# Performance work log

Measured on AMD Instinct MI355X. Metric: run time of the kernel, lower is better.

The kernel has to match this reference:

```python
import jax, jax.numpy as jnp
import numpy as np

TEMPERATURE = 12.5      # EMDLayer temperature
SINKHORN_EPS = 0.05     # entropic regularization for the batched EMD solve
SINKHORN_ITERS = 50     # fixed iteration count (jit-friendly)
WEIGHT_EPS = 1e-05      # OpenCVSolver adds 1e-5 after relu


def setup_inputs() -> dict:
    key = jax.random.key(0)
    k1, k2, k3 = jax.random.split(key, 3)
    E, Q, W, N = 4, 75, 5, 64
    similarity_map = jax.random.uniform(k1, (E, Q, W, N, N), dtype=jnp.float32)
    weight_1 = jax.random.uniform(k2, (E, Q, W, N), dtype=jnp.float32)
    weight_2 = jax.random.uniform(k3, (E, W, Q, N), dtype=jnp.float32)
    return {"similarity_map": similarity_map, "weight_1": weight_1, "weight_2": weight_2}


def _emd_flow(cost, a, b):
    """Batched entropic-regularized EMD (log-domain Sinkhorn).
    cost: [B, N, N]; a, b: [B, N] positive marginals (each sums to N).
    Returns flow: [B, N, N] with row sums ~a and col sums ~b."""
    logK = -cost / SINKHORN_EPS            # [B, N, N]
    log_a = jnp.log(a)
    log_b = jnp.log(b)

    def step(carry, _):
        log_u, log_v = carry
        log_u = log_a - jax.scipy.special.logsumexp(logK + log_v[:, None, :], axis=2)
        log_v = log_b - jax.scipy.special.logsumexp(logK + log_u[:, :, None], axis=1)
        return (log_u, log_v), None

    init = (jnp.zeros_like(log_a), jnp.zeros_like(log_b))
    (log_u, log_v), _ = jax.lax.scan(step, init, None, length=SINKHORN_ITERS)
    return jnp.exp(logK + log_u[:, :, None] + log_v[:, None, :])


def reference(similarity_map, weight_1, weight_2):
    E, Q, W, N, _ = similarity_map.shape
    sim = similarity_map.reshape(-1, N, N)                       # [B, N, N]
    w1 = weight_1.reshape(-1, N)                                  # [B, N]
    w2 = jnp.transpose(weight_2, (0, 2, 1, 3)).reshape(-1, N)     # transpose(1,2) then flatten

    # OpenCVSolver weight preprocessing: relu + eps, renormalize to sum N
    w1 = jax.nn.relu(w1) + WEIGHT_EPS
    w1 = w1 * (N / jnp.sum(w1, axis=1, keepdims=True))
    w2 = jax.nn.relu(w2) + WEIGHT_EPS
    w2 = w2 * (N / jnp.sum(w2, axis=1, keepdims=True))

    cost = 1.0 - sim
    flow = _emd_flow(cost, w1, w2)                                # [B, N, N]
    scores = jnp.sum(flow * sim, axis=(-1, -2)).reshape(E, Q, W)
    return scores * (TEMPERATURE / N)
```

## Files before the change

### kernel.cpp

```cpp
#include <hip/hip_runtime.h>

#define N 64
#define NPAD 65
#define ITERS 50
#define TEMP 12.5f
#define WEPS 1e-5f
#define QDIM 75
#define WDIM 5

__device__ __forceinline__ float rl(float x, int lane) {
    return __int_as_float(__builtin_amdgcn_readlane(__float_as_int(x), lane));
}

__device__ __forceinline__ float waveReduceSum(float x) {
#pragma unroll
    for (int off = 32; off; off >>= 1) x += __shfl_xor(x, off, 64);
    return x;
}

__global__ __launch_bounds__(64, 1) void emd_sinkhorn_kernel(
    const float* __restrict__ sim,
    const float* __restrict__ w1,
    const float* __restrict__ w2,
    float* __restrict__ out,
    int B)
{
    __shared__ float S[N * NPAD];

    const int b    = blockIdx.x;
    const int lane = threadIdx.x;
    const float* g = sim + (size_t)b * N * N;

    const float4* g4 = (const float4*)g;
#pragma unroll
    for (int t = 0; t < 16; ++t) {
        float4 x = g4[t * 64 + lane];
        int idx = t * 64 + lane;
        int r = idx >> 4;
        int c = (idx & 15) * 4;
        S[r * NPAD + c + 0] = x.x;
        S[r * NPAD + c + 1] = x.y;
        S[r * NPAD + c + 2] = x.z;
        S[r * NPAD + c + 3] = x.w;
    }
    __syncthreads();

    float Krow[N], Kcol[N];
#pragma unroll
    for (int j = 0; j < N; ++j)
        Krow[j] = __expf((S[lane * NPAD + j] - 1.0f) * 20.0f);
#pragma unroll
    for (int i = 0; i < N; ++i)
        Kcol[i] = __expf((S[i * NPAD + lane] - 1.0f) * 20.0f);

#pragma unroll
    for (int j = 0; j < N; ++j) {
        asm volatile("" : "+v"(Krow[j]));
        asm volatile("" : "+v"(Kcol[j]));
    }

    float a = w1[(size_t)b * N + lane];
    a = fmaxf(a, 0.0f) + WEPS;
    a *= (float)N / waveReduceSum(a);

    const int e   = b / (QDIM * WDIM);
    const int rem = b % (QDIM * WDIM);
    const int q   = rem / WDIM;
    const int w   = rem % WDIM;
    float bb = w2[((((size_t)e * WDIM + w) * QDIM) + q) * N + lane];
    bb = fmaxf(bb, 0.0f) + WEPS;
    bb *= (float)N / waveReduceSum(bb);

    float v = 1.0f, u = 0.0f;
#pragma unroll 1
    for (int it = 0; it < ITERS; ++it) {
        float c0 = 0, c1 = 0, c2 = 0, c3 = 0, c4 = 0, c5 = 0, c6 = 0, c7 = 0;
#pragma unroll
        for (int j = 0; j < N; j += 8) {
            c0 = fmaf(Krow[j + 0], rl(v, j + 0), c0);
            c1 = fmaf(Krow[j + 1], rl(v, j + 1), c1);
            c2 = fmaf(Krow[j + 2], rl(v, j + 2), c2);
            c3 = fmaf(Krow[j + 3], rl(v, j + 3), c3);
            c4 = fmaf(Krow[j + 4], rl(v, j + 4), c4);
            c5 = fmaf(Krow[j + 5], rl(v, j + 5), c5);
            c6 = fmaf(Krow[j + 6], rl(v, j + 6), c6);
            c7 = fmaf(Krow[j + 7], rl(v, j + 7), c7);
        }
        u = a * __builtin_amdgcn_rcpf(((c0 + c1) + (c2 + c3)) + ((c4 + c5) + (c6 + c7)));

        float d0 = 0, d1 = 0, d2 = 0, d3 = 0, d4 = 0, d5 = 0, d6 = 0, d7 = 0;
#pragma unroll
        for (int i = 0; i < N; i += 8) {
            d0 = fmaf(Kcol[i + 0], rl(u, i + 0), d0);
            d1 = fmaf(Kcol[i + 1], rl(u, i + 1), d1);
            d2 = fmaf(Kcol[i + 2], rl(u, i + 2), d2);
            d3 = fmaf(Kcol[i + 3], rl(u, i + 3), d3);
            d4 = fmaf(Kcol[i + 4], rl(u, i + 4), d4);
            d5 = fmaf(Kcol[i + 5], rl(u, i + 5), d5);
            d6 = fmaf(Kcol[i + 6], rl(u, i + 6), d6);
            d7 = fmaf(Kcol[i + 7], rl(u, i + 7), d7);
        }
        v = bb * __builtin_amdgcn_rcpf(((d0 + d1) + (d2 + d3)) + ((d4 + d5) + (d6 + d7)));
    }

    float s0 = 0, s1 = 0, s2 = 0, s3 = 0;
#pragma unroll
    for (int j = 0; j < N; j += 4) {
        s0 = fmaf(Krow[j + 0] * S[lane * NPAD + j + 0], rl(v, j + 0), s0);
        s1 = fmaf(Krow[j + 1] * S[lane * NPAD + j + 1], rl(v, j + 1), s1);
        s2 = fmaf(Krow[j + 2] * S[lane * NPAD + j + 2], rl(v, j + 2), s2);
        s3 = fmaf(Krow[j + 3] * S[lane * NPAD + j + 3], rl(v, j + 3), s3);
    }
    float partial = u * ((s0 + s1) + (s2 + s3));
    float tot = waveReduceSum(partial);
    if (lane == 0) out[b] = tot * (TEMP / (float)N);
}

extern "C" void kernel_launch(void* const* d_in, const int* in_sizes, int n_in,
                              void* d_out, int out_size, void* d_ws, size_t ws_size,
                              hipStream_t stream) {
    const float* sim = (const float*)d_in[0];
    const float* w1  = (const float*)d_in[1];
    const float* w2  = (const float*)d_in[2];
    float* out       = (float*)d_out;
    const int B = in_sizes[0] / (N * N);
    emd_sinkhorn_kernel<<<B, 64, 0, stream>>>(sim, w1, w2, out, B);
}
```

Baseline: 111.2 us.

## Process two Sinkhorn problems per wave and broadcast scalings via LDS

Each 64-thread block now solves two batch elements at once, keeping row and column kernels for both in registers (256 floats per lane). The per-iteration u/v broadcasts move from readlane instructions to LDS float4 broadcast reads with block barriers. The intent is to interleave two independent dependency chains for more instruction-level parallelism and to drop the scalar readlane traffic. In exchange, register pressure roughly doubles, which risks spills, and there are extra LDS round-trips and syncs per iteration.

```diff
diff --git a/kernel.cpp b/kernel.cpp
--- a/kernel.cpp
+++ b/kernel.cpp
@@ -8,112 +8,163 @@
 #define QDIM 75
 #define WDIM 5
 
-__device__ __forceinline__ float rl(float x, int lane) {
-    return __int_as_float(__builtin_amdgcn_readlane(__float_as_int(x), lane));
-}
-
 __device__ __forceinline__ float waveReduceSum(float x) {
 #pragma unroll
     for (int off = 32; off; off >>= 1) x += __shfl_xor(x, off, 64);
     return x;
 }
 
-__global__ __launch_bounds__(64, 1) void emd_sinkhorn_kernel(
+__global__ __launch_bounds__(64, 1) void emd_sinkhorn2(
     const float* __restrict__ sim,
     const float* __restrict__ w1,
     const float* __restrict__ w2,
     float* __restrict__ out,
     int B)
 {
-    __shared__ float S[N * NPAD];
+    __shared__ float S0[N * NPAD];
+    __shared__ float S1[N * NPAD];
+    __shared__ __align__(16) float U0[N], V0[N], U1[N], V1[N];
 
-    const int b    = blockIdx.x;
     const int lane = threadIdx.x;
-    const float* g = sim + (size_t)b * N * N;
+    const int b0 = blockIdx.x * 2;
+    const int b1e = b0 + 1;
+    const int b1 = (b1e < B) ? b1e : b0;
 
-    const float4* g4 = (const float4*)g;
+    {
+        const float4* g40 = (const float4*)(sim + (size_t)b0 * N * N);
+        const float4* g41 = (const float4*)(sim + (size_t)b1 * N * N);
 #pragma unroll
-    for (int t = 0; t < 16; ++t) {
-        float4 x = g4[t * 64 + lane];
-        int idx = t * 64 + lane;
-        int r = idx >> 4;
-        int c = (idx & 15) * 4;
-        S[r * NPAD + c + 0] = x.x;
-        S[r * NPAD + c + 1] = x.y;
-        S[r * NPAD + c + 2] = x.z;
-        S[r * NPAD + c + 3] = x.w;
+        for (int t = 0; t < 16; ++t) {
+            float4 x = g40[t * 64 + lane];
+            float4 y = g41[t * 64 + lane];
+            int idx = t * 64 + lane;
+            int r = idx >> 4;
+            int c = (idx & 15) * 4;
+            S0[r * NPAD + c + 0] = x.x;  S0[r * NPAD + c + 1] = x.y;
+            S0[r * NPAD + c + 2] = x.z;  S0[r * NPAD + c + 3] = x.w;
+            S1[r * NPAD + c + 0] = y.x;  S1[r * NPAD + c + 1] = y.y;
+            S1[r * NPAD + c + 2] = y.z;  S1[r * NPAD + c + 3] = y.w;
+        }
     }
     __syncthreads();
 
-    float Krow[N], Kcol[N];
-#pragma unroll
-    for (int j = 0; j < N; ++j)
-        Krow[j] = __expf((S[lane * NPAD + j] - 1.0f) * 20.0f);
-#pragma unroll
-    for (int i = 0; i < N; ++i)
-        Kcol[i] = __expf((S[i * NPAD + lane] - 1.0f) * 20.0f);
-
+    float K0r[N], K0c[N], K1r[N], K1c[N];
 #pragma unroll
     for (int j = 0; j < N; ++j) {
-        asm volatile("" : "+v"(Krow[j]));
-        asm volatile("" : "+v"(Kcol[j]));
+        K0r[j] = __expf((S0[lane * NPAD + j] - 1.0f) * 20.0f);
+        K1r[j] = __expf((S1[lane * NPAD + j] - 1.0f) * 20.0f);
+    }
+#pragma unroll
+    for (int i = 0; i < N; ++i) {
+        K0c[i] = __expf((S0[i * NPAD + lane] - 1.0f) * 20.0f);
+        K1c[i] = __expf((S1[i * NPAD + lane] - 1.0f) * 20.0f);
+    }
+#pragma unroll
+    for (int j = 0; j < N; ++j) {
+        asm volatile("" : "+v"(K0r[j]));
+        asm volatile("" : "+v"(K0c[j]));
+        asm volatile("" : "+v"(K1r[j]));
+        asm volatile("" : "+v"(K1c[j]));
     }
 
-    float a = w1[(size_t)b * N + lane];
-    a = fmaxf(a, 0.0f) + WEPS;
-    a *= (float)N / waveReduceSum(a);
+    float a0 = w1[(size_t)b0 * N + lane];
+    a0 = fmaxf(a0, 0.0f) + WEPS;
+    a0 *= (float)N / waveReduceSum(a0);
+    float a1 = w1[(size_t)b1 * N + lane];
+    a1 = fmaxf(a1, 0.0f) + WEPS;
+    a1 *= (float)N / waveReduceSum(a1);
 
-    const int e   = b / (QDIM * WDIM);
-    const int rem = b % (QDIM * WDIM);
-    const int q   = rem / WDIM;
-    const int w   = rem % WDIM;
-    float bb = w2[((((size_t)e * WDIM + w) * QDIM) + q) * N + lane];
-    bb = fmaxf(bb, 0.0f) + WEPS;
-    bb *= (float)N / waveReduceSum(bb);
+    int e = b0 / (QDIM * WDIM), rem = b0 % (QDIM * WDIM);
+    int q = rem / WDIM, w = rem % WDIM;
+    float g0 = w2[((((size_t)e * WDIM + w) * QDIM) + q) * N + lane];
+    g0 = fmaxf(g0, 0.0f) + WEPS;
+    g0 *= (float)N / waveReduceSum(g0);
 
-    float v = 1.0f, u = 0.0f;
+    e = b1 / (QDIM * WDIM); rem = b1 % (QDIM * WDIM);
+    q = rem / WDIM; w = rem % WDIM;
+    float g1 = w2[((((size_t)e * WDIM + w) * QDIM) + q) * N + lane];
+    g1 = fmaxf(g1, 0.0f) + WEPS;
+    g1 *= (float)N / waveReduceSum(g1);
+
+    V0[lane] = 1.0f;
+    V1[lane] = 1.0f;
+    __syncthreads();
+
+    float u0 = 0.0f, u1 = 0.0f;
 #pragma unroll 1
     for (int it = 0; it < ITERS; ++it) {
-        float c0 = 0, c1 = 0, c2 = 0, c3 = 0, c4 = 0, c5 = 0, c6 = 0, c7 = 0;
+        {
+            const float4* A4 = (const float4*)V0;
+            const float4* B4 = (const float4*)V1;
+            float p0 = 0, p1 = 0, p2 = 0, p3 = 0, p4 = 0, p5 = 0, p6 = 0, p7 = 0;
+            float r0 = 0, r1 = 0, r2 = 0, r3 = 0, r4 = 0, r5 = 0, r6 = 0, r7 = 0;
 #pragma unroll
-        for (int j = 0; j < N; j += 8) {
-            c0 = fmaf(Krow[j + 0], rl(v, j + 0), c0);
-            c1 = fmaf(Krow[j + 1], rl(v, j + 1), c1);
-            c2 = fmaf(Krow[j + 2], rl(v, j + 2), c2);
-            c3 = fmaf(Krow[j + 3], rl(v, j + 3), c3);
-            c4 = fmaf(Krow[j + 4], rl(v, j + 4), c4);
-            c5 = fmaf(Krow[j + 5], rl(v, j + 5), c5);
-            c6 = fmaf(Krow[j + 6], rl(v, j + 6), c6);
-            c7 = fmaf(Krow[j + 7], rl(v, j + 7), c7);
+            for (int j8 = 0; j8 < 8; ++j8) {
+                float4 x0 = A4[2 * j8], x1 = A4[2 * j8 + 1];
+                float4 y0 = B4[2 * j8], y1 = B4[2 * j8 + 1];
+                p0 = fmaf(K0r[8 * j8 + 0], x0.x, p0);  r0 = fmaf(K1r[8 * j8 + 0], y0.x, r0);
+                p1 = fmaf(K0r[8 * j8 + 1], x0.y, p1);  r1 = fmaf(K1r[8 * j8 + 1], y0.y, r1);
+                p2 = fmaf(K0r[8 * j8 + 2], x0.z, p2);  r2 = fmaf(K1r[8 * j8 + 2], y0.z, r2);
+                p3 = fmaf(K0r[8 * j8 + 3], x0.w, p3);  r3 = fmaf(K1r[8 * j8 + 3], y0.w, r3);
+                p4 = fmaf(K0r[8 * j8 + 4], x1.x, p4);  r4 = fmaf(K1r[8 * j8 + 4], y1.x, r4);
+                p5 = fmaf(K0r[8 * j8 + 5], x1.y, p5);  r5 = fmaf(K1r[8 * j8 + 5], y1.y, r5);
+                p6 = fmaf(K0r[8 * j8 + 6], x1.z, p6);  r6 = fmaf(K1r[8 * j8 + 6], y1.z, r6);
+                p7 = fmaf(K0r[8 * j8 + 7], x1.w, p7);  r7 = fmaf(K1r[8 * j8 + 7], y1.w, r7);
+            }
+            u0 = a0 * __builtin_amdgcn_rcpf(((p0 + p1) + (p2 + p3)) + ((p4 + p5) + (p6 + p7)));
+            u1 = a1 * __builtin_amdgcn_rcpf(((r0 + r1) + (r2 + r3)) + ((r4 + r5) + (r6 + r7)));
+            U0[lane] = u0;
+            U1[lane] = u1;
         }
-        u = a * __builtin_amdgcn_rcpf(((c0 + c1) + (c2 + c3)) + ((c4 + c5) + (c6 + c7)));
+        __syncthreads();
 
-        float d0 = 0, d1 = 0, d2 = 0, d3 = 0, d4 = 0, d5 = 0, d6 = 0, d7 = 0;
+        {
+            const float4* A4 = (const float4*)U0;
+            const float4* B4 = (const float4*)U1;
+            float p0 = 0, p1 = 0, p2 = 0, p3 = 0, p4 = 0, p5 = 0, p6 = 0, p7 = 0;
+            float r0 = 0, r1 = 0, r2 = 0, r3 = 0, r4 = 0, r5 = 0, r6 = 0, r7 = 0;
 #pragma unroll
-        for (int i = 0; i < N; i += 8) {
-            d0 = fmaf(Kcol[i + 0], rl(u, i + 0), d0);
-            d1 = fmaf(Kcol[i + 1], rl(u, i + 1), d1);
-            d2 = fmaf(Kcol[i + 2], rl(u, i + 2), d2);
-            d3 = fmaf(Kcol[i + 3], rl(u, i + 3), d3);
-            d4 = fmaf(Kcol[i + 4], rl(u, i + 4), d4);
-            d5 = fmaf(Kcol[i + 5], rl(u, i + 5), d5);
-            d6 = fmaf(Kcol[i + 6], rl(u, i + 6), d6);
-            d7 = fmaf(Kcol[i + 7], rl(u, i + 7), d7);
+            for (int i8 = 0; i8 < 8; ++i8) {
+                float4 x0 = A4[2 * i8], x1 = A4[2 * i8 + 1];
+                float4 y0 = B4[2 * i8], y1 = B4[2 * i8 + 1];
+                p0 = fmaf(K0c[8 * i8 + 0], x0.x, p0);  r0 = fmaf(K1c[8 * i8 + 0], y0.x, r0);
+                p1 = fmaf(K0c[8 * i8 + 1], x0.y, p1);  r1 = fmaf(K1c[8 * i8 + 1], y0.y, r1);
+                p2 = fmaf(K0c[8 * i8 + 2], x0.z, p2);  r2 = fmaf(K1c[8 * i8 + 2], y0.z, r2);
+                p3 = fmaf(K0c[8 * i8 + 3], x0.w, p3);  r3 = fmaf(K1c[8 * i8 + 3], y0.w, r3);
+                p4 = fmaf(K0c[8 * i8 + 4], x1.x, p4);  r4 = fmaf(K1c[8 * i8 + 4], y1.x, r4);
+                p5 = fmaf(K0c[8 * i8 + 5], x1.y, p5);  r5 = fmaf(K1c[8 * i8 + 5], y1.y, r5);
+                p6 = fmaf(K0c[8 * i8 + 6], x1.z, p6);  r6 = fmaf(K1c[8 * i8 + 6], y1.z, r6);
+                p7 = fmaf(K0c[8 * i8 + 7], x1.w, p7);  r7 = fmaf(K1c[8 * i8 + 7], y1.w, r7);
+            }
+            float v0 = g0 * __builtin_amdgcn_rcpf(((p0 + p1) + (p2 + p3)) + ((p4 + p5) + (p6 + p7)));
+            float v1 = g1 * __builtin_amdgcn_rcpf(((r0 + r1) + (r2 + r3)) + ((r4 + r5) + (r6 + r7)));
+            V0[lane] = v0;
+            V1[lane] = v1;
         }
-        v = bb * __builtin_amdgcn_rcpf(((d0 + d1) + (d2 + d3)) + ((d4 + d5) + (d6 + d7)));
+        __syncthreads();
     }
 
     float s0 = 0, s1 = 0, s2 = 0, s3 = 0;
+    float t0 = 0, t1 = 0, t2 = 0, t3 = 0;
 #pragma unroll
-    for (int j = 0; j < N; j += 4) {
-        s0 = fmaf(Krow[j + 0] * S[lane * NPAD + j + 0], rl(v, j + 0), s0);
-        s1 = fmaf(Krow[j + 1] * S[lane * NPAD + j + 1], rl(v, j + 1), s1);
-        s2 = fmaf(Krow[j + 2] * S[lane * NPAD + j + 2], rl(v, j + 2), s2);
-        s3 = fmaf(Krow[j + 3] * S[lane * NPAD + j + 3], rl(v, j + 3), s3);
+    for (int j4 = 0; j4 < 16; ++j4) {
+        float4 x = ((const float4*)V0)[j4];
+        float4 y = ((const float4*)V1)[j4];
+        s0 = fmaf(K0r[4 * j4 + 0] * S0[lane * NPAD + 4 * j4 + 0], x.x, s0);
+        s1 = fmaf(K0r[4 * j4 + 1] * S0[lane * NPAD + 4 * j4 + 1], x.y, s1);
+        s2 = fmaf(K0r[4 * j4 + 2] * S0[lane * NPAD + 4 * j4 + 2], x.z, s2);
+        s3 = fmaf(K0r[4 * j4 + 3] * S0[lane * NPAD + 4 * j4 + 3], x.w, s3);
+        t0 = fmaf(K1r[4 * j4 + 0] * S1[lane * NPAD + 4 * j4 + 0], y.x, t0);
+        t1 = fmaf(K1r[4 * j4 + 1] * S1[lane * NPAD + 4 * j4 + 1], y.y, t1);
+        t2 = fmaf(K1r[4 * j4 + 2] * S1[lane * NPAD + 4 * j4 + 2], y.z, t2);
+        t3 = fmaf(K1r[4 * j4 + 3] * S1[lane * NPAD + 4 * j4 + 3], y.w, t3);
     }
-    float partial = u * ((s0 + s1) + (s2 + s3));
-    float tot = waveReduceSum(partial);
-    if (lane == 0) out[b] = tot * (TEMP / (float)N);
+    float tot0 = waveReduceSum(u0 * ((s0 + s1) + (s2 + s3)));
+    float tot1 = waveReduceSum(u1 * ((t0 + t1) + (t2 + t3)));
+    if (lane == 0) {
+        out[b0] = tot0 * (TEMP / (float)N);
+        if (b1e < B) out[b1e] = tot1 * (TEMP / (float)N);
+    }
 }
 
 extern "C" void kernel_launch(void* const* d_in, const int* in_sizes, int n_in,
@@ -124,5 +175,6 @@
     const float* w2  = (const float*)d_in[2];
     float* out       = (float*)d_out;
     const int B = in_sizes[0] / (N * N);
-    emd_sinkhorn_kernel<<<B, 64, 0, stream>>>(sim, w1, w2, out, B);
+    const int nb = (B + 1) / 2;
+    emd_sinkhorn2<<<nb, 64, 0, stream>>>(sim, w1, w2, out, B);
 }
```

New measurement: 156.3 us. 40.5% more time.

## Replace readlane broadcasts with systolic DPP wave rotations in Sinkhorn matvecs

Applied to the files above, without the earlier changes.

Swaps the per-element v_readlane broadcasts in both Sinkhorn matrix-vector products for a systolic scheme. The vector rotates around the wave with DPP wave_rol/wave_ror in two directions, and each lane holds its K entries pre-permuted to match the rotation order. The final score recovers sim from log2(K), so the sim values no longer need to be read back from LDS. This targets the scalar readlane bottleneck, but it leaves two serial dependency chains of 32 DPP ops per matvec, and the log-based reconstruction can lose accuracy for very small K.

```diff
diff --git a/kernel.cpp b/kernel.cpp
--- a/kernel.cpp
+++ b/kernel.cpp
@@ -8,9 +8,8 @@
 #define QDIM 75
 #define WDIM 5
 
-__device__ __forceinline__ float rl(float x, int lane) {
-    return __int_as_float(__builtin_amdgcn_readlane(__float_as_int(x), lane));
-}
+#define ROL(x) __int_as_float(__builtin_amdgcn_update_dpp(0, __float_as_int(x), 0x134, 0xF, 0xF, true))
+#define ROR(x) __int_as_float(__builtin_amdgcn_update_dpp(0, __float_as_int(x), 0x13C, 0xF, 0xF, true))
 
 __device__ __forceinline__ float waveReduceSum(float x) {
 #pragma unroll
@@ -18,7 +17,7 @@
     return x;
 }
 
-__global__ __launch_bounds__(64, 1) void emd_sinkhorn_kernel(
+__global__ __launch_bounds__(64, 1) void emd_systolic(
     const float* __restrict__ sim,
     const float* __restrict__ w1,
     const float* __restrict__ w2,
@@ -27,11 +26,14 @@
 {
     __shared__ float S[N * NPAD];
 
+    const int lane = threadIdx.x;
     const int b    = blockIdx.x;
-    const int lane = threadIdx.x;
-    const float* g = sim + (size_t)b * N * N;
+    const float* gm = sim + (size_t)b * N * N;
 
-    const float4* g4 = (const float4*)g;
+    const int dl = (__builtin_amdgcn_update_dpp(0, lane, 0x134, 0xF, 0xF, true) - lane) & 63;
+    const int dr = (__builtin_amdgcn_update_dpp(0, lane, 0x13C, 0xF, 0xF, true) - lane) & 63;
+
+    const float4* g4 = (const float4*)gm;
 #pragma unroll
     for (int t = 0; t < 16; ++t) {
         float4 x = g4[t * 64 + lane];
@@ -45,75 +47,87 @@
     }
     __syncthreads();
 
-    float Krow[N], Kcol[N];
+    float KL[32], KR[32], CL[32], CR[32];
 #pragma unroll
-    for (int j = 0; j < N; ++j)
-        Krow[j] = __expf((S[lane * NPAD + j] - 1.0f) * 20.0f);
+    for (int m = 0; m < 32; ++m) {
+        int cL = (lane + dl * m) & 63;
+        int cR = (lane + dr * (m + 1)) & 63;
+        KL[m] = __expf((S[lane * NPAD + cL] - 1.0f) * 20.0f);
+        KR[m] = __expf((S[lane * NPAD + cR] - 1.0f) * 20.0f);
+        CL[m] = __expf((S[cL * NPAD + lane] - 1.0f) * 20.0f);
+        CR[m] = __expf((S[cR * NPAD + lane] - 1.0f) * 20.0f);
+    }
 #pragma unroll
-    for (int i = 0; i < N; ++i)
-        Kcol[i] = __expf((S[i * NPAD + lane] - 1.0f) * 20.0f);
-
-#pragma unroll
-    for (int j = 0; j < N; ++j) {
-        asm volatile("" : "+v"(Krow[j]));
-        asm volatile("" : "+v"(Kcol[j]));
+    for (int m = 0; m < 32; ++m) {
+        asm volatile("" : "+v"(KL[m]));
+        asm volatile("" : "+v"(KR[m]));
+        asm volatile("" : "+v"(CL[m]));
+        asm volatile("" : "+v"(CR[m]));
     }
 
-    float a = w1[(size_t)b * N + lane];
-    a = fmaxf(a, 0.0f) + WEPS;
-    a *= (float)N / waveReduceSum(a);
+    float a_own = w1[(size_t)b * N + lane];
+    a_own = fmaxf(a_own, 0.0f) + WEPS;
+    a_own *= (float)N / waveReduceSum(a_own);
 
-    const int e   = b / (QDIM * WDIM);
-    const int rem = b % (QDIM * WDIM);
-    const int q   = rem / WDIM;
-    const int w   = rem % WDIM;
-    float bb = w2[((((size_t)e * WDIM + w) * QDIM) + q) * N + lane];
-    bb = fmaxf(bb, 0.0f) + WEPS;
-    bb *= (float)N / waveReduceSum(bb);
+    const int e  = b / (QDIM * WDIM);
+    const int rm = b % (QDIM * WDIM);
+    const int q  = rm / WDIM, w = rm % WDIM;
+    float b_own = w2[((((size_t)e * WDIM + w) * QDIM) + q) * N + lane];
+    b_own = fmaxf(b_own, 0.0f) + WEPS;
+    b_own *= (float)N / waveReduceSum(b_own);
 
-    float v = 1.0f, u = 0.0f;
+    float vv = 1.0f, u = 0.0f;
 #pragma unroll 1
     for (int it = 0; it < ITERS; ++it) {
-        float c0 = 0, c1 = 0, c2 = 0, c3 = 0, c4 = 0, c5 = 0, c6 = 0, c7 = 0;
+        {
+            float wL = vv, wR = vv;
+            float accL = KL[0] * wL;
+            float accR = 0.0f;
 #pragma unroll
-        for (int j = 0; j < N; j += 8) {
-            c0 = fmaf(Krow[j + 0], rl(v, j + 0), c0);
-            c1 = fmaf(Krow[j + 1], rl(v, j + 1), c1);
-            c2 = fmaf(Krow[j + 2], rl(v, j + 2), c2);
-            c3 = fmaf(Krow[j + 3], rl(v, j + 3), c3);
-            c4 = fmaf(Krow[j + 4], rl(v, j + 4), c4);
-            c5 = fmaf(Krow[j + 5], rl(v, j + 5), c5);
-            c6 = fmaf(Krow[j + 6], rl(v, j + 6), c6);
-            c7 = fmaf(Krow[j + 7], rl(v, j + 7), c7);
+            for (int m = 1; m <= 32; ++m) {
+                wR = ROR(wR);
+                accR = fmaf(KR[m - 1], wR, accR);
+                if (m <= 31) {
+                    wL = ROL(wL);
+                    accL = fmaf(KL[m], wL, accL);
+                }
+            }
+            u = a_own * __builtin_amdgcn_rcpf(accL + accR);
         }
-        u = a * __builtin_amdgcn_rcpf(((c0 + c1) + (c2 + c3)) + ((c4 + c5) + (c6 + c7)));
-
-        float d0 = 0, d1 = 0, d2 = 0, d3 = 0, d4 = 0, d5 = 0, d6 = 0, d7 = 0;
+        {
+            float wL = u, wR = u;
+            float accL = CL[0] * wL;
+            float accR = 0.0f;
 #pragma unroll
-        for (int i = 0; i < N; i += 8) {
-            d0 = fmaf(Kcol[i + 0], rl(u, i + 0), d0);
-            d1 = fmaf(Kcol[i + 1], rl(u, i + 1), d1);
-            d2 = fmaf(Kcol[i + 2], rl(u, i + 2), d2);
-            d3 = fmaf(Kcol[i + 3], rl(u, i + 3), d3);
-            d4 = fmaf(Kcol[i + 4], rl(u, i + 4), d4);
-            d5 = fmaf(Kcol[i + 5], rl(u, i + 5), d5);
-            d6 = fmaf(Kcol[i + 6], rl(u, i + 6), d6);
-            d7 = fmaf(Kcol[i + 7], rl(u, i + 7), d7);
+            for (int m = 1; m <= 32; ++m) {
+                wR = ROR(wR);
+                accR = fmaf(CR[m - 1], wR, accR);
+                if (m <= 31) {
+                    wL = ROL(wL);
+                    accL = fmaf(CL[m], wL, accL);
+                }
+            }
+            vv = b_own * __builtin_amdgcn_rcpf(accL + accR);
         }
-        v = bb * __builtin_amdgcn_rcpf(((d0 + d1) + (d2 + d3)) + ((d4 + d5) + (d6 + d7)));
     }
 
-    float s0 = 0, s1 = 0, s2 = 0, s3 = 0;
+    {
+        const float cc = 0.69314718056f / 20.0f;
+        float wL = vv, wR = vv;
+        float sL = KL[0] * fmaf(__log2f(KL[0]), cc, 1.0f) * wL;
+        float sR = 0.0f;
 #pragma unroll
-    for (int j = 0; j < N; j += 4) {
-        s0 = fmaf(Krow[j + 0] * S[lane * NPAD + j + 0], rl(v, j + 0), s0);
-        s1 = fmaf(Krow[j + 1] * S[lane * NPAD + j + 1], rl(v, j + 1), s1);
-        s2 = fmaf(Krow[j + 2] * S[lane * NPAD + j + 2], rl(v, j + 2), s2);
-        s3 = fmaf(Krow[j + 3] * S[lane * NPAD + j + 3], rl(v, j + 3), s3);
+        for (int m = 1; m <= 32; ++m) {
+            wR = ROR(wR);
+            sR = fmaf(KR[m - 1] * fmaf(__log2f(KR[m - 1]), cc, 1.0f), wR, sR);
+            if (m <= 31) {
+                wL = ROL(wL);
+                sL = fmaf(KL[m] * fmaf(__log2f(KL[m]), cc, 1.0f), wL, sL);
+            }
+        }
+        float tot = waveReduceSum(u * (sL + sR));
+        if (lane == 0) out[b] = tot * (TEMP / (float)N);
     }
-    float partial = u * ((s0 + s1) + (s2 + s3));
-    float tot = waveReduceSum(partial);
-    if (lane == 0) out[b] = tot * (TEMP / (float)N);
 }
 
 extern "C" void kernel_launch(void* const* d_in, const int* in_sizes, int n_in,
@@ -124,5 +138,5 @@
     const float* w2  = (const float*)d_in[2];
     float* out       = (float*)d_out;
     const int B = in_sizes[0] / (N * N);
-    emd_sinkhorn_kernel<<<B, 64, 0, stream>>>(sim, w1, w2, out, B);
+    emd_systolic<<<B, 64, 0, stream>>>(sim, w1, w2, out, B);
 }
```

Measured after the change: 111.5 us. No clear change (+0.3%).
